# Kernel tuning notes

Measured on AMD Instinct MI355X. Metric: run time of the kernel, lower is better.

## Reference

```python
import jax, jax.numpy as jnp
import numpy as np

EMBED_DIM = 512
VIR_HEADS = 8


def _make_buffers():
    # angle: 1/10000**linspace(0,1,embed//H//2), each entry repeated twice (rotary pairs)
    half = EMBED_DIM // VIR_HEADS // 2
    angle = 1.0 / 10000 ** jnp.linspace(0.0, 1.0, half)
    angle = jnp.repeat(angle, 2)  # [head_dim]
    decay = jnp.log(1 - 2 ** (-2 - 5 * jnp.arange(VIR_HEADS, dtype=jnp.float32) / VIR_HEADS))
    return angle.astype(jnp.float32), decay.astype(jnp.float32)


def setup_inputs() -> dict:
    key = jax.random.key(0)
    B, H, N1, N2 = 8, 8, 32, 32
    offsets = jax.random.normal(key, (B, H, N1, N2, 2), dtype=jnp.float32)
    angle, decay = _make_buffers()
    return {"slen": N1 * N2, "offsets": offsets, "angle": angle, "decay": decay}


def reference(slen, offsets, angle, decay):
    B, H, N1, N2, _ = offsets.shape
    idx1 = jnp.arange(N1, dtype=offsets.dtype)
    idx2 = jnp.arange(N2, dtype=offsets.dtype)

    # key-side rotary phases: index_k[i*N2+j] = i + j
    index_k = (idx1[:, None] + idx2[None, :]).reshape(slen)  # [slen]
    phase_k = index_k[:, None] * angle[None, :]               # [slen, D]
    sin_k, cos_k = jnp.sin(phase_k), jnp.cos(phase_k)

    # query-side deformed indices
    index1_q = idx1.reshape(1, 1, N1, 1) + offsets[..., 0]    # [B,H,N1,N2]
    index2_q = idx2.reshape(1, 1, 1, N2) + offsets[..., 1]    # [B,H,N1,N2]
    index_q = (index1_q + index2_q).reshape(B, H, slen, 1)    # [B,H,slen,1]
    phase_q = index_q * angle.reshape(1, 1, 1, -1)            # [B,H,slen,D]
    sin_q, cos_q = jnp.sin(phase_q), jnp.cos(phase_q)

    # L1 distance between deformed query position and each key grid position
    d1 = jnp.abs(index1_q[..., None, None] - idx1.reshape(1, 1, 1, 1, N1, 1))  # [B,H,N1,N2,N1,1]
    d2 = jnp.abs(index2_q[..., None, None] - idx2.reshape(1, 1, 1, 1, 1, N2))  # [B,H,N1,N2,1,N2]
    mask = (d1 + d2).reshape(B, H, slen, slen)
    mask = jnp.exp(mask * decay[None, :, None, None])
    mask = jnp.nan_to_num(mask)
    mask = mask / jnp.sqrt(jnp.sum(mask, axis=-1, keepdims=True))
    return sin_q, cos_q, sin_k, cos_k, mask
```

## Files before the change

kernel.cpp:

```cpp
#include <hip/hip_runtime.h>
#include <math.h>

#define OFF_COSQ  4194304
#define OFF_SINK  8388608
#define OFF_COSK  8454144
#define OFF_MASK  8519680
#define NROWS     65536

typedef float floatx4 __attribute__((ext_vector_type(4)));

__global__ __launch_bounds__(256) void retnet_fused_kernel(
    const float* __restrict__ offsets,
    const float* __restrict__ angle,
    const float* __restrict__ decay,
    float* __restrict__ out)
{
    const int wave = blockIdx.x * 4 + (threadIdx.x >> 6);
    const int lane = threadIdx.x & 63;

    const int bh = wave >> 10;
    const int s  = wave & 1023;
    const int h  = bh & 7;
    const int i  = s >> 5;
    const int j  = s & 31;

    const float off0 = offsets[(wave << 1) + 0];
    const float off1 = offsets[(wave << 1) + 1];
    const float i1q  = (float)i + off0;
    const float i2q  = (float)j + off1;
    const float dec  = decay[h];
    const float ang  = angle[lane];

    {
        float sq, cq;
        __sincosf((i1q + i2q) * ang, &sq, &cq);
        __builtin_nontemporal_store(sq, &out[(size_t)wave * 64 + lane]);
        __builtin_nontemporal_store(cq, &out[OFF_COSQ + (size_t)wave * 64 + lane]);
    }

    if (bh == 0) {
        float sk, ck;
        __sincosf((float)(i + j) * ang, &sk, &ck);
        __builtin_nontemporal_store(sk, &out[OFF_SINK + (size_t)s * 64 + lane]);
        __builtin_nontemporal_store(ck, &out[OFF_COSK + (size_t)s * 64 + lane]);
    }

    const int   l5   = lane & 31;
    const float base = (lane < 32) ? i1q : i2q;
    const float v    = __expf(dec * fabsf(base - (float)l5));

    float sum = v;
    #pragma unroll
    for (int m = 16; m >= 1; m >>= 1) sum += __shfl_xor(sum, m, 64);
    const float sum1 = __shfl(sum, 0, 64);
    const float sum2 = __shfl(sum, 32, 64);
    const float invnorm = rsqrtf(sum1 * sum2);

    const float vs = (lane < 32) ? v * invnorm : v;

    const int jj0 = (lane & 7) * 4;
    floatx4 e2q;
    e2q.x = __shfl(vs, 32 + jj0 + 0, 64);
    e2q.y = __shfl(vs, 32 + jj0 + 1, 64);
    e2q.z = __shfl(vs, 32 + jj0 + 2, 64);
    e2q.w = __shfl(vs, 32 + jj0 + 3, 64);

    const int ii0 = lane >> 3;
    float e1a[4];
    #pragma unroll
    for (int k = 0; k < 4; ++k) e1a[k] = __shfl(vs, k * 8 + ii0, 64);

    floatx4* mrow = (floatx4*)(out + OFF_MASK + (size_t)wave * 1024);
    #pragma unroll
    for (int k = 0; k < 4; ++k) {
        floatx4 r = e2q * e1a[k];
        __builtin_nontemporal_store(r, &mrow[k * 64 + lane]);
    }
}

extern "C" void kernel_launch(void* const* d_in, const int* in_sizes, int n_in,
                              void* d_out, int out_size, void* d_ws, size_t ws_size,
                              hipStream_t stream) {
    const float* offsets = (const float*)d_in[1];
    const float* angle   = (const float*)d_in[2];
    const float* decay   = (const float*)d_in[3];
    float* out = (float*)d_out;

    const int blocks = NROWS / 4;
    retnet_fused_kernel<<<blocks, 256, 0, stream>>>(offsets, angle, decay, out);
}
```

Baseline: 302.2 us.

## Process four rows per wave and recompute mask factors instead of shuffling

Each wave now handles four consecutive query rows, with the launch grid shrunk to match, so per-wave setup is amortised and independent reductions can interleave. The mask factors that were broadcast across lanes with shuffles are now recomputed per lane with extra exp calls, trading shuffle latency for transcendental work. The kernel is dominated by writing the large mask output, so gains depend on whether fewer, heavier waves still keep enough stores in flight.

```diff
diff --git a/kernel.cpp b/kernel.cpp
--- a/kernel.cpp
+++ b/kernel.cpp
@@ -6,6 +6,7 @@
 #define OFF_COSK  8454144
 #define OFF_MASK  8519680
 #define NROWS     65536
+#define ROWS_PER_WAVE 4
 
 typedef float floatx4 __attribute__((ext_vector_type(4)));
 
@@ -17,64 +18,87 @@
 {
     const int wave = blockIdx.x * 4 + (threadIdx.x >> 6);
     const int lane = threadIdx.x & 63;
+    const int r0   = wave * ROWS_PER_WAVE;
 
-    const int bh = wave >> 10;
-    const int s  = wave & 1023;
+    const int bh = r0 >> 10;
     const int h  = bh & 7;
-    const int i  = s >> 5;
-    const int j  = s & 31;
+    const float dec = decay[h];
+    const float ang = angle[lane];
 
-    const float off0 = offsets[(wave << 1) + 0];
-    const float off1 = offsets[(wave << 1) + 1];
-    const float i1q  = (float)i + off0;
-    const float i2q  = (float)j + off1;
-    const float dec  = decay[h];
-    const float ang  = angle[lane];
+    float i1q[ROWS_PER_WAVE], i2q[ROWS_PER_WAVE];
+    #pragma unroll
+    for (int t = 0; t < ROWS_PER_WAVE; ++t) {
+        const int r = r0 + t;
+        const int s = r & 1023;
+        const int i = s >> 5;
+        const int j = s & 31;
+        i1q[t] = (float)i + offsets[(r << 1) + 0];
+        i2q[t] = (float)j + offsets[(r << 1) + 1];
+    }
 
-    {
+    #pragma unroll
+    for (int t = 0; t < ROWS_PER_WAVE; ++t) {
+        const int r = r0 + t;
         float sq, cq;
-        __sincosf((i1q + i2q) * ang, &sq, &cq);
-        __builtin_nontemporal_store(sq, &out[(size_t)wave * 64 + lane]);
-        __builtin_nontemporal_store(cq, &out[OFF_COSQ + (size_t)wave * 64 + lane]);
+        __sincosf((i1q[t] + i2q[t]) * ang, &sq, &cq);
+        __builtin_nontemporal_store(sq, &out[(size_t)r * 64 + lane]);
+        __builtin_nontemporal_store(cq, &out[OFF_COSQ + (size_t)r * 64 + lane]);
     }
 
     if (bh == 0) {
-        float sk, ck;
-        __sincosf((float)(i + j) * ang, &sk, &ck);
-        __builtin_nontemporal_store(sk, &out[OFF_SINK + (size_t)s * 64 + lane]);
-        __builtin_nontemporal_store(ck, &out[OFF_COSK + (size_t)s * 64 + lane]);
+        #pragma unroll
+        for (int t = 0; t < ROWS_PER_WAVE; ++t) {
+            const int s = r0 + t;
+            const int i = s >> 5;
+            const int j = s & 31;
+            float sk, ck;
+            __sincosf((float)(i + j) * ang, &sk, &ck);
+            __builtin_nontemporal_store(sk, &out[OFF_SINK + (size_t)s * 64 + lane]);
+            __builtin_nontemporal_store(ck, &out[OFF_COSK + (size_t)s * 64 + lane]);
+        }
     }
 
-    const int   l5   = lane & 31;
-    const float base = (lane < 32) ? i1q : i2q;
-    const float v    = __expf(dec * fabsf(base - (float)l5));
-
-    float sum = v;
-    #pragma unroll
-    for (int m = 16; m >= 1; m >>= 1) sum += __shfl_xor(sum, m, 64);
-    const float sum1 = __shfl(sum, 0, 64);
-    const float sum2 = __shfl(sum, 32, 64);
-    const float invnorm = rsqrtf(sum1 * sum2);
-
-    const float vs = (lane < 32) ? v * invnorm : v;
+    float invnorm[ROWS_PER_WAVE];
+    {
+        const int l5 = lane & 31;
+        float v[ROWS_PER_WAVE], sum[ROWS_PER_WAVE];
+        #pragma unroll
+        for (int t = 0; t < ROWS_PER_WAVE; ++t) {
+            const float base = (lane < 32) ? i1q[t] : i2q[t];
+            v[t]   = __expf(dec * fabsf(base - (float)l5));
+            sum[t] = v[t];
+        }
+        #pragma unroll
+        for (int m = 16; m >= 1; m >>= 1) {
+            #pragma unroll
+            for (int t = 0; t < ROWS_PER_WAVE; ++t)
+                sum[t] += __shfl_xor(sum[t], m, 64);
+        }
+        #pragma unroll
+        for (int t = 0; t < ROWS_PER_WAVE; ++t) {
+            const float s1 = __shfl(sum[t], 0, 64);
+            const float s2 = __shfl(sum[t], 32, 64);
+            invnorm[t] = rsqrtf(s1 * s2);
+        }
+    }
 
     const int jj0 = (lane & 7) * 4;
-    floatx4 e2q;
-    e2q.x = __shfl(vs, 32 + jj0 + 0, 64);
-    e2q.y = __shfl(vs, 32 + jj0 + 1, 64);
-    e2q.z = __shfl(vs, 32 + jj0 + 2, 64);
-    e2q.w = __shfl(vs, 32 + jj0 + 3, 64);
+    const int ii0 = lane >> 3;
+    #pragma unroll
+    for (int t = 0; t < ROWS_PER_WAVE; ++t) {
+        const int r = r0 + t;
+        floatx4 e2q;
+        e2q.x = __expf(dec * fabsf(i2q[t] - (float)(jj0 + 0))) * invnorm[t];
+        e2q.y = __expf(dec * fabsf(i2q[t] - (float)(jj0 + 1))) * invnorm[t];
+        e2q.z = __expf(dec * fabsf(i2q[t] - (float)(jj0 + 2))) * invnorm[t];
+        e2q.w = __expf(dec * fabsf(i2q[t] - (float)(jj0 + 3))) * invnorm[t];
 
-    const int ii0 = lane >> 3;
-    float e1a[4];
-    #pragma unroll
-    for (int k = 0; k < 4; ++k) e1a[k] = __shfl(vs, k * 8 + ii0, 64);
-
-    floatx4* mrow = (floatx4*)(out + OFF_MASK + (size_t)wave * 1024);
-    #pragma unroll
-    for (int k = 0; k < 4; ++k) {
-        floatx4 r = e2q * e1a[k];
-        __builtin_nontemporal_store(r, &mrow[k * 64 + lane]);
+        floatx4* mrow = (floatx4*)(out + OFF_MASK + (size_t)r * 1024);
+        #pragma unroll
+        for (int k = 0; k < 4; ++k) {
+            const float e1 = __expf(dec * fabsf(i1q[t] - (float)(k * 8 + ii0)));
+            __builtin_nontemporal_store(e2q * e1, &mrow[k * 64 + lane]);
+        }
     }
 }
 
@@ -86,6 +110,6 @@
     const float* decay   = (const float*)d_in[3];
     float* out = (float*)d_out;
 
-    const int blocks = NROWS / 4;
+    const int blocks = NROWS / ROWS_PER_WAVE / 4;
     retnet_fused_kernel<<<blocks, 256, 0, stream>>>(offsets, angle, decay, out);
 }
```

Result: no change. 304.3 us (+0.7%).
